# Kernel optimization log

Measured on AMD Instinct MI355X. Metric: run time of the kernel, lower is better.

The kernel has to match this reference:

```python
import jax, jax.numpy as jnp
import numpy as np

N, C_IN, H, W = 1024, 22, 19, 19
C_TRUNK, HID, NHIST = 384, 128, 5
HIST_START = 9  # channels 9..13 hold move history planes


def setup_inputs() -> dict:
    key = jax.random.key(0)
    ks = jax.random.split(key, 8)
    return {
        "input_spatial": jax.random.uniform(ks[0], (N, C_IN, H, W), dtype=jnp.float32),
        "trunk_out": jax.random.normal(ks[1], (N, C_TRUNK, H, W), dtype=jnp.float32),
        "w_ih": jax.random.normal(ks[2], (4 * HID, C_TRUNK), dtype=jnp.float32) * 0.05,
        "w_hh": jax.random.normal(ks[3], (4 * HID, HID), dtype=jnp.float32) * 0.05,
        "b_ih": jax.random.normal(ks[4], (4 * HID,), dtype=jnp.float32) * 0.05,
        "b_hh": jax.random.normal(ks[5], (4 * HID,), dtype=jnp.float32) * 0.05,
        "w_proj": jax.random.normal(ks[6], (C_TRUNK, HID), dtype=jnp.float32) * 0.05,
        "b_proj": jax.random.normal(ks[7], (C_TRUNK,), dtype=jnp.float32) * 0.05,
    }


def reference(input_spatial, trunk_out, w_ih, w_hh, b_ih, b_hh, w_proj, b_proj):
    n, _, h, w = input_spatial.shape
    c_trunk = trunk_out.shape[1]
    # --- extract_move_coords (vectorized) ---
    planes = input_spatial[:, HIST_START:HIST_START + NHIST]          # N,5,H,W
    flat = planes.reshape(n, NHIST, h * w)                            # N,5,HW
    has_move = flat.sum(axis=-1) > 0.5                                # N,5 bool
    idx = jnp.argmax(flat, axis=-1)                                   # N,5 (== r*W+c; clamp(-1,min=0)==0 handled by mask)
    # --- gather trunk features at move coords, mask missing moves ---
    trunk_flat = trunk_out.reshape(n, c_trunk, h * w)                 # N,Ct,HW
    feats = jnp.take_along_axis(trunk_flat, idx[:, None, :], axis=2)  # N,Ct,5
    feats = feats.transpose(0, 2, 1) * has_move[..., None].astype(trunk_out.dtype)  # N,5,Ct
    seq = feats[:, ::-1, :]                                           # oldest -> newest
    # --- single-layer LSTM (torch gate order: i, f, g, o) ---
    def step(carry, x_t):
        h_t, c_t = carry
        g = x_t @ w_ih.T + h_t @ w_hh.T + b_ih + b_hh                 # N,4H
        i_g, f_g, g_g, o_g = jnp.split(g, 4, axis=-1)
        c_new = jax.nn.sigmoid(f_g) * c_t + jax.nn.sigmoid(i_g) * jnp.tanh(g_g)
        h_new = jax.nn.sigmoid(o_g) * jnp.tanh(c_new)
        return (h_new, c_new), None

    h0 = jnp.zeros((n, HID), dtype=seq.dtype)
    (h_final, _), _ = jax.lax.scan(step, (h0, h0), seq.transpose(1, 0, 2))
    out = h_final @ w_proj.T + b_proj                                 # N,Ct
    return out[:, :, None, None]                                      # N,Ct,1,1
```

## Files before the change

kernel.cpp:

```cpp
#include <hip/hip_runtime.h>
#include <hip/hip_bf16.h>
#include <float.h>

#define N_SAMP   1024
#define C_IN     22
#define HW       361
#define C_TRUNK  384
#define HID      128
#define NHIST    5
#define HIST_START 9
#define NGATE    512

typedef __attribute__((ext_vector_type(8))) short short8v;
typedef __attribute__((ext_vector_type(4))) float float4v;

static __device__ __forceinline__ ushort f2bf(float x) {
  unsigned int b = __float_as_uint(x);
  b += 0x7fffu + ((b >> 16) & 1u);
  return (ushort)(b >> 16);
}

__global__ __launch_bounds__(320) void argmax_kernel(
    const float* __restrict__ inp,
    const float* __restrict__ w_ih,
    int*    __restrict__ idxb,
    float*  __restrict__ movb,
    ushort* __restrict__ w_ihb)
{
  const int n    = blockIdx.x;
  const int tid  = threadIdx.x;
  const int wave = tid >> 6;
  const int lane = tid & 63;

  if (n < 768 && tid < 256) {
    int o = n * 256 + tid;
    w_ihb[o] = f2bf(w_ih[o]);
  }

  const float* base = inp + ((size_t)n * C_IN + HIST_START + wave) * HW;
  float v = -FLT_MAX; int vi = 0; float sum = 0.f;
  #pragma unroll
  for (int r = 0; r < 6; ++r) {
    int i = lane + r * 64;
    if (i < HW) {
      float x = base[i];
      sum += x;
      if (x > v) { v = x; vi = i; }
    }
  }
  #pragma unroll
  for (int m = 1; m < 64; m <<= 1) {
    float v2 = __shfl_xor(v, m);
    int   i2 = __shfl_xor(vi, m);
    float s2 = __shfl_xor(sum, m);
    if (v2 > v || (v2 == v && i2 < vi)) { v = v2; vi = i2; }
    sum += s2;
  }
  if (lane == 0) {
    idxb[n * NHIST + wave] = vi;
    movb[n * NHIST + wave] = (sum > 0.5f) ? 1.f : 0.f;
  }
}

__global__ __launch_bounds__(192) void gather_kernel(
    const float* __restrict__ trunk,
    const int*   __restrict__ idxb,
    const float* __restrict__ movb,
    ushort* __restrict__ seq)
{
  const int n = blockIdx.x;
  const int c = threadIdx.x;

  const int   i0 = idxb[n * NHIST + 4], i1 = idxb[n * NHIST + 3],
              i2 = idxb[n * NHIST + 2], i3 = idxb[n * NHIST + 1],
              i4 = idxb[n * NHIST + 0];
  const float m0 = movb[n * NHIST + 4], m1 = movb[n * NHIST + 3],
              m2 = movb[n * NHIST + 2], m3 = movb[n * NHIST + 1],
              m4 = movb[n * NHIST + 0];

  const float* ta = trunk + ((size_t)n * C_TRUNK + c) * HW;
  const float* tb = ta + (size_t)192 * HW;
  float a0 = ta[i0], a1 = ta[i1], a2 = ta[i2], a3 = ta[i3], a4 = ta[i4];
  float b0 = tb[i0], b1 = tb[i1], b2 = tb[i2], b3 = tb[i3], b4 = tb[i4];

  ushort* so = seq + (size_t)n * NHIST * C_TRUNK + c;
  so[0 * C_TRUNK]       = f2bf(a0 * m0);
  so[1 * C_TRUNK]       = f2bf(a1 * m1);
  so[2 * C_TRUNK]       = f2bf(a2 * m2);
  so[3 * C_TRUNK]       = f2bf(a3 * m3);
  so[4 * C_TRUNK]       = f2bf(a4 * m4);
  so[0 * C_TRUNK + 192] = f2bf(b0 * m0);
  so[1 * C_TRUNK + 192] = f2bf(b1 * m1);
  so[2 * C_TRUNK + 192] = f2bf(b2 * m2);
  so[3 * C_TRUNK + 192] = f2bf(b3 * m3);
  so[4 * C_TRUNK + 192] = f2bf(b4 * m4);
}

__global__ __launch_bounds__(256) void gates_kernel(
    const ushort* __restrict__ seq,
    const ushort* __restrict__ w_ihb,
    const float*  __restrict__ b_ih,
    const float*  __restrict__ b_hh,
    float* __restrict__ G)
{
  __shared__ ushort As[64][40];
  __shared__ ushort Bs[64][40];
  const int tid  = threadIdx.x;
  const int wv   = tid >> 6;
  const int lane = tid & 63;
  const int m0 = blockIdx.y * 64;
  const int j0 = blockIdx.x * 64;
  const int row_l = tid >> 2;
  const int koff  = (tid & 3) * 8;

  float4v acc0 = {0.f,0.f,0.f,0.f};
  float4v acc1 = {0.f,0.f,0.f,0.f};
  float4v acc2 = {0.f,0.f,0.f,0.f};
  float4v acc3 = {0.f,0.f,0.f,0.f};

  const int fr = lane & 15;
  const int fk = (lane >> 4) * 8;

  for (int k0 = 0; k0 < C_TRUNK; k0 += 32) {
    *(short8v*)&As[row_l][koff] =
        *(const short8v*)(seq + (size_t)(m0 + row_l) * C_TRUNK + k0 + koff);
    *(short8v*)&Bs[row_l][koff] =
        *(const short8v*)(w_ihb + (size_t)(j0 + row_l) * C_TRUNK + k0 + koff);
    __syncthreads();

    short8v af  = *(const short8v*)&As[wv * 16 + fr][fk];
    short8v bf0 = *(const short8v*)&Bs[ 0 + fr][fk];
    short8v bf1 = *(const short8v*)&Bs[16 + fr][fk];
    short8v bf2 = *(const short8v*)&Bs[32 + fr][fk];
    short8v bf3 = *(const short8v*)&Bs[48 + fr][fk];
    acc0 = __builtin_amdgcn_mfma_f32_16x16x32_bf16(af, bf0, acc0, 0, 0, 0);
    acc1 = __builtin_amdgcn_mfma_f32_16x16x32_bf16(af, bf1, acc1, 0, 0, 0);
    acc2 = __builtin_amdgcn_mfma_f32_16x16x32_bf16(af, bf2, acc2, 0, 0, 0);
    acc3 = __builtin_amdgcn_mfma_f32_16x16x32_bf16(af, bf3, acc3, 0, 0, 0);
    __syncthreads();
  }

  const int rbase = m0 + wv * 16 + (lane >> 4) * 4;
  #pragma unroll
  for (int j = 0; j < 4; ++j) {
    const float4v a = (j == 0) ? acc0 : (j == 1) ? acc1 : (j == 2) ? acc2 : acc3;
    const int cj = j0 + j * 16 + fr;
    const float bsum = b_ih[cj] + b_hh[cj];
    #pragma unroll
    for (int r = 0; r < 4; ++r)
      G[(size_t)(rbase + r) * NGATE + cj] = a[r] + bsum;
  }
}

__global__ __launch_bounds__(512, 2) void lstm_kernel(
    const float* __restrict__ G,
    const float* __restrict__ w_hh,
    const float* __restrict__ w_proj,
    const float* __restrict__ b_proj,
    float* __restrict__ out)
{
  const int n0  = blockIdx.x * 4;
  const int tid = threadIdx.x;
  const int g   = tid >> 7;
  const int j   = tid & 127;

  __shared__ float hs[4][HID];
  __shared__ float glds[4][4][HID];

  float gpre[NHIST][4];
  #pragma unroll
  for (int t = 0; t < NHIST; ++t)
    #pragma unroll
    for (int s = 0; s < 4; ++s)
      gpre[t][s] = G[((size_t)(n0 + s) * NHIST + t) * NGATE + tid];

  float4 wreg[32];
  #pragma unroll
  for (int k4 = 0; k4 < 32; ++k4)
    wreg[k4] = *(const float4*)(w_hh + (size_t)(g * HID + j) * HID + k4 * 4);

  hs[g][j] = 0.f;
  float c = 0.f;
  __syncthreads();

  #pragma unroll
  for (int t = 0; t < NHIST; ++t) {
    float a[4];
    #pragma unroll
    for (int s = 0; s < 4; ++s) a[s] = gpre[t][s];

    #pragma unroll
    for (int k4 = 0; k4 < 32; ++k4) {
      float4 w = wreg[k4];
      #pragma unroll
      for (int s = 0; s < 4; ++s) {
        float4 h = *(const float4*)&hs[s][k4 * 4];
        a[s] += w.x * h.x + w.y * h.y + w.z * h.z + w.w * h.w;
      }
    }
    #pragma unroll
    for (int s = 0; s < 4; ++s) glds[g][s][j] = a[s];
    __syncthreads();
    {
      float ig = glds[0][g][j];
      float fg = glds[1][g][j];
      float gg = glds[2][g][j];
      float og = glds[3][g][j];
      ig = 1.f / (1.f + __expf(-ig));
      fg = 1.f / (1.f + __expf(-fg));
      og = 1.f / (1.f + __expf(-og));
      c  = fg * c + ig * tanhf(gg);
      hs[g][j] = og * tanhf(c);
    }
    __syncthreads();
  }

  if (tid < C_TRUNK) {
    const int cc = tid;
    const float4* wp = (const float4*)(w_proj + (size_t)cc * HID);
    float b = b_proj[cc];
    float po[4] = {b, b, b, b};
    #pragma unroll 8
    for (int k4 = 0; k4 < 32; ++k4) {
      float4 w  = wp[k4];
      float4 h0 = *(const float4*)&hs[0][k4 * 4];
      float4 h1 = *(const float4*)&hs[1][k4 * 4];
      float4 h2 = *(const float4*)&hs[2][k4 * 4];
      float4 h3 = *(const float4*)&hs[3][k4 * 4];
      po[0] += w.x*h0.x + w.y*h0.y + w.z*h0.z + w.w*h0.w;
      po[1] += w.x*h1.x + w.y*h1.y + w.z*h1.z + w.w*h1.w;
      po[2] += w.x*h2.x + w.y*h2.y + w.z*h2.z + w.w*h2.w;
      po[3] += w.x*h3.x + w.y*h3.y + w.z*h3.z + w.w*h3.w;
    }
    #pragma unroll
    for (int s = 0; s < 4; ++s)
      out[(size_t)(n0 + s) * C_TRUNK + cc] = po[s];
  }
}

extern "C" void kernel_launch(void* const* d_in, const int* in_sizes, int n_in,
                              void* d_out, int out_size, void* d_ws, size_t ws_size,
                              hipStream_t stream) {
  const float* inp    = (const float*)d_in[0];
  const float* trunk  = (const float*)d_in[1];
  const float* w_ih   = (const float*)d_in[2];
  const float* w_hh   = (const float*)d_in[3];
  const float* b_ih   = (const float*)d_in[4];
  const float* b_hh   = (const float*)d_in[5];
  const float* w_proj = (const float*)d_in[6];
  const float* b_proj = (const float*)d_in[7];
  float* out = (float*)d_out;

  char* ws = (char*)d_ws;
  int*    idxb  = (int*)ws;
  float*  movb  = (float*)(ws + 20480);
  ushort* w_ihb = (ushort*)(ws + 40960);
  ushort* seq   = (ushort*)(ws + 40960 + 393216);
  float*  G     = (float*)(ws + 40960 + 393216 +
                   (size_t)N_SAMP * NHIST * C_TRUNK * sizeof(ushort));

  argmax_kernel<<<N_SAMP, 320, 0, stream>>>(inp, w_ih, idxb, movb, w_ihb);
  gather_kernel<<<N_SAMP, 192, 0, stream>>>(trunk, idxb, movb, seq);
  gates_kernel<<<dim3(NGATE / 64, (N_SAMP * NHIST) / 64), 256, 0, stream>>>(
      seq, w_ihb, b_ih, b_hh, G);
  lstm_kernel<<<N_SAMP / 4, 512, 0, stream>>>(G, w_hh, w_proj, b_proj, out);
}
```

Before: 81.21 us.

## Use bf16 MFMA for LSTM recurrent matmul and output projection

The recurrent h@W_hh product and the final projection now run on 16x16x32 bf16 MFMA instructions. The fp32 FMA loops over register-held weights are gone. Hidden state is kept in LDS in a swizzled bf16 layout that matches the A-fragment, with only 4 of 16 rows used, and the gate nonlinearities are computed by 128 threads over 4 samples each. This cuts VALU work and register pressure, but it adds bf16 rounding of h and the weights, idles most threads during the elementwise phase, and leaves most of the MFMA rows as padding.

```diff
diff --git a/kernel.cpp b/kernel.cpp
--- a/kernel.cpp
+++ b/kernel.cpp
@@ -159,82 +159,129 @@
     const float* __restrict__ b_proj,
     float* __restrict__ out)
 {
-  const int n0  = blockIdx.x * 4;
-  const int tid = threadIdx.x;
-  const int g   = tid >> 7;
-  const int j   = tid & 127;
-
-  __shared__ float hs[4][HID];
-  __shared__ float glds[4][4][HID];
-
-  float gpre[NHIST][4];
+  const int n0   = blockIdx.x * 4;
+  const int tid  = threadIdx.x;
+  const int wv   = tid >> 6;
+  const int lane = tid & 63;
+  const int fr   = lane & 15;
+  const int fq   = lane >> 4;
+
+  __shared__ ushort hswz[4][64][8];
+  __shared__ float  glds[NGATE][4];
+
+  ((ushort4*)hswz)[tid] = make_ushort4(0, 0, 0, 0);
+
+  const int j0w = wv * 64;
+  short8v bfrag[4][4];
+  #pragma unroll
+  for (int f = 0; f < 4; ++f)
+    #pragma unroll
+    for (int ks = 0; ks < 4; ++ks) {
+      const float* wr = w_hh + (size_t)(j0w + f*16 + fr) * HID + ks*32 + fq*8;
+      float4 lo = *(const float4*)wr;
+      float4 hi = *(const float4*)(wr + 4);
+      short8v b;
+      b[0]=(short)f2bf(lo.x); b[1]=(short)f2bf(lo.y);
+      b[2]=(short)f2bf(lo.z); b[3]=(short)f2bf(lo.w);
+      b[4]=(short)f2bf(hi.x); b[5]=(short)f2bf(hi.y);
+      b[6]=(short)f2bf(hi.z); b[7]=(short)f2bf(hi.w);
+      bfrag[f][ks] = b;
+    }
+
+  float4v gpre[NHIST][4];
   #pragma unroll
   for (int t = 0; t < NHIST; ++t)
     #pragma unroll
-    for (int s = 0; s < 4; ++s)
-      gpre[t][s] = G[((size_t)(n0 + s) * NHIST + t) * NGATE + tid];
-
-  float4 wreg[32];
-  #pragma unroll
-  for (int k4 = 0; k4 < 32; ++k4)
-    wreg[k4] = *(const float4*)(w_hh + (size_t)(g * HID + j) * HID + k4 * 4);
-
-  hs[g][j] = 0.f;
-  float c = 0.f;
+    for (int f = 0; f < 4; ++f) {
+      float4v v = {0.f, 0.f, 0.f, 0.f};
+      if (fq == 0) {
+        const int col = j0w + f*16 + fr;
+        #pragma unroll
+        for (int r = 0; r < 4; ++r)
+          v[r] = G[((size_t)(n0 + r) * NHIST + t) * NGATE + col];
+      }
+      gpre[t][f] = v;
+    }
+
+  float c4[4] = {0.f, 0.f, 0.f, 0.f};
   __syncthreads();
 
   #pragma unroll
   for (int t = 0; t < NHIST; ++t) {
-    float a[4];
-    #pragma unroll
-    for (int s = 0; s < 4; ++s) a[s] = gpre[t][s];
-
-    #pragma unroll
-    for (int k4 = 0; k4 < 32; ++k4) {
-      float4 w = wreg[k4];
+    short8v af0 = *(const short8v*)&hswz[0][lane][0];
+    short8v af1 = *(const short8v*)&hswz[1][lane][0];
+    short8v af2 = *(const short8v*)&hswz[2][lane][0];
+    short8v af3 = *(const short8v*)&hswz[3][lane][0];
+    #pragma unroll
+    for (int f = 0; f < 4; ++f) {
+      float4v acc = gpre[t][f];
+      acc = __builtin_amdgcn_mfma_f32_16x16x32_bf16(af0, bfrag[f][0], acc, 0, 0, 0);
+      acc = __builtin_amdgcn_mfma_f32_16x16x32_bf16(af1, bfrag[f][1], acc, 0, 0, 0);
+      acc = __builtin_amdgcn_mfma_f32_16x16x32_bf16(af2, bfrag[f][2], acc, 0, 0, 0);
+      acc = __builtin_amdgcn_mfma_f32_16x16x32_bf16(af3, bfrag[f][3], acc, 0, 0, 0);
+      if (fq == 0)
+        *(float4v*)&glds[j0w + f*16 + fr][0] = acc;
+    }
+    __syncthreads();
+
+    if (tid < HID) {
+      const int j = tid;
+      float4 iv = *(const float4*)&glds[      j][0];
+      float4 fv = *(const float4*)&glds[128 + j][0];
+      float4 gv = *(const float4*)&glds[256 + j][0];
+      float4 ov = *(const float4*)&glds[384 + j][0];
+      float ia[4] = {iv.x, iv.y, iv.z, iv.w};
+      float fa[4] = {fv.x, fv.y, fv.z, fv.w};
+      float ga[4] = {gv.x, gv.y, gv.z, gv.w};
+      float oa[4] = {ov.x, ov.y, ov.z, ov.w};
       #pragma unroll
       for (int s = 0; s < 4; ++s) {
-        float4 h = *(const float4*)&hs[s][k4 * 4];
-        a[s] += w.x * h.x + w.y * h.y + w.z * h.z + w.w * h.w;
+        float ig = 1.f / (1.f + __expf(-ia[s]));
+        float fg = 1.f / (1.f + __expf(-fa[s]));
+        float og = 1.f / (1.f + __expf(-oa[s]));
+        c4[s] = fg * c4[s] + ig * tanhf(ga[s]);
+        float h = og * tanhf(c4[s]);
+        hswz[j >> 5][((j >> 3) & 3) * 16 + s][j & 7] = f2bf(h);
       }
     }
-    #pragma unroll
-    for (int s = 0; s < 4; ++s) glds[g][s][j] = a[s];
     __syncthreads();
-    {
-      float ig = glds[0][g][j];
-      float fg = glds[1][g][j];
-      float gg = glds[2][g][j];
-      float og = glds[3][g][j];
-      ig = 1.f / (1.f + __expf(-ig));
-      fg = 1.f / (1.f + __expf(-fg));
-      og = 1.f / (1.f + __expf(-og));
-      c  = fg * c + ig * tanhf(gg);
-      hs[g][j] = og * tanhf(c);
-    }
-    __syncthreads();
-  }
-
-  if (tid < C_TRUNK) {
-    const int cc = tid;
-    const float4* wp = (const float4*)(w_proj + (size_t)cc * HID);
-    float b = b_proj[cc];
-    float po[4] = {b, b, b, b};
-    #pragma unroll 8
-    for (int k4 = 0; k4 < 32; ++k4) {
-      float4 w  = wp[k4];
-      float4 h0 = *(const float4*)&hs[0][k4 * 4];
-      float4 h1 = *(const float4*)&hs[1][k4 * 4];
-      float4 h2 = *(const float4*)&hs[2][k4 * 4];
-      float4 h3 = *(const float4*)&hs[3][k4 * 4];
-      po[0] += w.x*h0.x + w.y*h0.y + w.z*h0.z + w.w*h0.w;
-      po[1] += w.x*h1.x + w.y*h1.y + w.z*h1.z + w.w*h1.w;
-      po[2] += w.x*h2.x + w.y*h2.y + w.z*h2.z + w.w*h2.w;
-      po[3] += w.x*h3.x + w.y*h3.y + w.z*h3.z + w.w*h3.w;
-    }
-    #pragma unroll
-    for (int s = 0; s < 4; ++s)
-      out[(size_t)(n0 + s) * C_TRUNK + cc] = po[s];
+  }
+
+  const int j0p = wv * 48;
+  short8v pfrag[3][4];
+  #pragma unroll
+  for (int f = 0; f < 3; ++f)
+    #pragma unroll
+    for (int ks = 0; ks < 4; ++ks) {
+      const float* wr = w_proj + (size_t)(j0p + f*16 + fr) * HID + ks*32 + fq*8;
+      float4 lo = *(const float4*)wr;
+      float4 hi = *(const float4*)(wr + 4);
+      short8v b;
+      b[0]=(short)f2bf(lo.x); b[1]=(short)f2bf(lo.y);
+      b[2]=(short)f2bf(lo.z); b[3]=(short)f2bf(lo.w);
+      b[4]=(short)f2bf(hi.x); b[5]=(short)f2bf(hi.y);
+      b[6]=(short)f2bf(hi.z); b[7]=(short)f2bf(hi.w);
+      pfrag[f][ks] = b;
+    }
+
+  short8v hf0 = *(const short8v*)&hswz[0][lane][0];
+  short8v hf1 = *(const short8v*)&hswz[1][lane][0];
+  short8v hf2 = *(const short8v*)&hswz[2][lane][0];
+  short8v hf3 = *(const short8v*)&hswz[3][lane][0];
+  #pragma unroll
+  for (int f = 0; f < 3; ++f) {
+    const int col = j0p + f * 16 + fr;
+    const float bp = b_proj[col];
+    float4v acc = {bp, bp, bp, bp};
+    acc = __builtin_amdgcn_mfma_f32_16x16x32_bf16(hf0, pfrag[f][0], acc, 0, 0, 0);
+    acc = __builtin_amdgcn_mfma_f32_16x16x32_bf16(hf1, pfrag[f][1], acc, 0, 0, 0);
+    acc = __builtin_amdgcn_mfma_f32_16x16x32_bf16(hf2, pfrag[f][2], acc, 0, 0, 0);
+    acc = __builtin_amdgcn_mfma_f32_16x16x32_bf16(hf3, pfrag[f][3], acc, 0, 0, 0);
+    if (fq == 0) {
+      #pragma unroll
+      for (int r = 0; r < 4; ++r)
+        out[(size_t)(n0 + r) * C_TRUNK + col] = acc[r];
+    }
   }
 }
 
```

Result: faster. 77.87 us (-4.1%).
